# Optimization experiments

Measured on AMD Instinct MI355X. Metric: run time of the kernel, lower is better.

Reference implementation:

```python
import jax, jax.numpy as jnp
import numpy as np

HIDDEN = 1152
HEADS = 16
HEAD_DIM = HIDDEN // HEADS

def setup_inputs() -> dict:
    key = jax.random.key(0)
    ks = jax.random.split(key, 7)
    s = 1.0 / np.sqrt(HIDDEN)
    return {
        "x": jax.random.normal(ks[0], (16, 1024, HIDDEN), dtype=jnp.float32),
        "w_qkv": jax.random.normal(ks[1], (3 * HIDDEN, HIDDEN), dtype=jnp.float32) * s,
        "b_qkv": jax.random.normal(ks[2], (3 * HIDDEN,), dtype=jnp.float32) * 0.01,
        "q_gamma": jnp.ones((HEAD_DIM,), dtype=jnp.float32),
        "k_gamma": jnp.ones((HEAD_DIM,), dtype=jnp.float32),
        "w_proj": jax.random.normal(ks[3], (HIDDEN, HIDDEN), dtype=jnp.float32) * s,
        "b_proj": jax.random.normal(ks[4], (HIDDEN,), dtype=jnp.float32) * 0.01,
    }

def _rmsnorm(t, gamma):
    # normalize over last dim (head_dim); torch RMSNorm default eps = finfo(dtype).eps
    eps = jnp.asarray(jnp.finfo(t.dtype).eps, t.dtype)
    ms = jnp.mean(jnp.square(t), axis=-1, keepdims=True)
    return t * jax.lax.rsqrt(ms + eps) * gamma

def reference(x, w_qkv, b_qkv, q_gamma, k_gamma, w_proj, b_proj):
    B, S, H = x.shape
    qkv = x @ w_qkv.T + b_qkv                       # [B,S,3H]
    qkv = qkv.reshape(B, S, 3, HEADS, HEAD_DIM)
    qkv = jnp.transpose(qkv, (2, 0, 3, 1, 4))       # [3,B,nh,S,hd]
    q, k, v = qkv[0], qkv[1], qkv[2]
    q = _rmsnorm(q, q_gamma)
    k = _rmsnorm(k, k_gamma)
    scale = 1.0 / np.sqrt(HEAD_DIM)
    scores = jnp.einsum('bhqd,bhkd->bhqk', q, k) * scale
    probs = jax.nn.softmax(scores, axis=-1)
    out = jnp.einsum('bhqk,bhkd->bhqd', probs, v)   # [B,nh,S,hd]
    out = jnp.transpose(out, (0, 2, 1, 3)).reshape(B, S, H)
    return out @ w_proj.T + b_proj
```

## Files before the change

kernel.cpp:

```cpp
#include <hip/hip_runtime.h>

typedef _Float16 f16;
typedef _Float16 f16x8 __attribute__((ext_vector_type(8)));
typedef _Float16 f16x4 __attribute__((ext_vector_type(4)));
typedef float f32x4 __attribute__((ext_vector_type(4)));

__device__ __forceinline__ void gld16(const void* g, void* l) {
    __builtin_amdgcn_global_load_lds(
        (const __attribute__((address_space(1))) void*)g,
        (__attribute__((address_space(3))) void*)l,
        16, 0, 0);
}

__global__ __launch_bounds__(256) void f32_to_f16_vec(const float* __restrict__ in,
                                                      f16* __restrict__ out, long n4) {
    long i = (long)blockIdx.x * 256 + threadIdx.x;
    if (i < n4) {
        float4 v = ((const float4*)in)[i];
        f16x4 o = {(f16)v.x, (f16)v.y, (f16)v.z, (f16)v.w};
        ((f16x4*)out)[i] = o;
    }
}

constexpr int GBUF = 24576;

template<int P, int KK, bool STG>
__device__ __forceinline__ void phase_step(f16* sm,
                                           const f16*& gSA, const f16*& gSB,
                                           long sKA, int dA, int dB,
                                           int rA, int rB,
                                           f32x4 (&acc)[4][4]) {
    const f16* ba = sm + P * GBUF + KK * 8192 + rA;
    const f16* bb = sm + P * GBUF + KK * 4096 + rB;
    f16x8 af[4], bf[4];
#pragma unroll
    for (int mt = 0; mt < 4; ++mt) af[mt] = *(const f16x8*)(ba + mt * 512);
#pragma unroll
    for (int nt = 0; nt < 4; ++nt) bf[nt] = *(const f16x8*)(bb + nt * 512);
    if (STG) {
        constexpr int TB = (KK == 0) ? (P ^ 1) : P;
        constexpr int TK = (KK == 0) ? 1 : 0;
        f16* d = sm + TB * GBUF;
        gld16(gSA,       d + TK * 8192 + dA);
        gld16(gSA + sKA, d + TK * 8192 + dA + 512);
        gld16(gSB,       d + 16384 + TK * 4096 + dB);
        gSA += 32; gSB += 32;
    }
    asm volatile("s_waitcnt lgkmcnt(0)" ::: "memory");
    __builtin_amdgcn_sched_barrier(0);
    __builtin_amdgcn_s_setprio(1);
#pragma unroll
    for (int mt = 0; mt < 4; ++mt)
#pragma unroll
        for (int nt = 0; nt < 4; ++nt)
            acc[mt][nt] = __builtin_amdgcn_mfma_f32_16x16x32_f16(
                af[mt], bf[nt], acc[mt][nt], 0, 0, 0);
    __builtin_amdgcn_s_setprio(0);
}

__global__ __launch_bounds__(512, 2) void gemm8(const f16* __restrict__ A,
                                                const f16* __restrict__ B,
                                                const float* __restrict__ bias,
                                                float* __restrict__ Cf,
                                                f16* __restrict__ Ch,
                                                int M, int N, int K) {
    __shared__ f16 sm[2 * GBUF];
    const int tid = threadIdx.x;
    const int w = tid >> 6, lane = tid & 63;
    const int quad = lane >> 4, l16 = lane & 15;
    const int wm = w >> 1, wn = w & 1;

    const int nnb = N >> 7;
    const int mpx = (M >> 8) >> 3;
    const int xcd = blockIdx.x & 7;
    const int s = blockIdx.x >> 3;
    const int mband = s / nnb;
    const int nblk = s - mband * nnb;
    const long m0 = (long)(xcd * mpx + mband) << 8;
    const long n0 = (long)nblk << 7;

    const int r4 = lane >> 2;
    const int scw = ((lane & 3) ^ ((lane >> 3) & 3)) << 3;
    const f16* gSA = A + (m0 + w * 32 + r4) * (long)K + scw;
    const f16* gSB = B + (n0 + w * 16 + r4) * (long)K + scw;
    const long sKA = (long)16 * K;
    const int dA = __builtin_amdgcn_readfirstlane(w * 1024);
    const int dB = __builtin_amdgcn_readfirstlane(w * 512);

    const int swz8 = (quad ^ ((l16 >> 1) & 3)) << 3;
    const int rA = (wm * 64 + l16) * 32 + swz8;
    const int rB = 16384 + (wn * 64 + l16) * 32 + swz8;

    f32x4 acc[4][4] = {};

    gld16(gSA, sm + dA); gld16(gSA + sKA, sm + dA + 512);
    gld16(gSB, sm + 16384 + dB); gSA += 32; gSB += 32;
    gld16(gSA, sm + 8192 + dA); gld16(gSA + sKA, sm + 8192 + dA + 512);
    gld16(gSB, sm + 20480 + dB); gSA += 32; gSB += 32;
    gld16(gSA, sm + GBUF + dA); gld16(gSA + sKA, sm + GBUF + dA + 512);
    gld16(gSB, sm + GBUF + 16384 + dB); gSA += 32; gSB += 32;
    asm volatile("s_waitcnt vmcnt(6)" ::: "memory");
    __builtin_amdgcn_s_barrier();

#define VMB(N) asm volatile("s_waitcnt vmcnt(" #N ")" ::: "memory"); \
               __builtin_amdgcn_s_barrier();

#pragma unroll 1
    for (int it = 0; it < 8; ++it) {
        phase_step<0, 0, true>(sm, gSA, gSB, sKA, dA, dB, rA, rB, acc); VMB(6)
        phase_step<0, 1, true>(sm, gSA, gSB, sKA, dA, dB, rA, rB, acc); VMB(6)
        phase_step<1, 0, true>(sm, gSA, gSB, sKA, dA, dB, rA, rB, acc); VMB(6)
        phase_step<1, 1, true>(sm, gSA, gSB, sKA, dA, dB, rA, rB, acc); VMB(6)
    }
    phase_step<0, 0, true >(sm, gSA, gSB, sKA, dA, dB, rA, rB, acc); VMB(6)
    phase_step<0, 1, false>(sm, gSA, gSB, sKA, dA, dB, rA, rB, acc); VMB(3)
    phase_step<1, 0, false>(sm, gSA, gSB, sKA, dA, dB, rA, rB, acc); VMB(0)
    phase_step<1, 1, false>(sm, gSA, gSB, sKA, dA, dB, rA, rB, acc);
#undef VMB

    float bv[4];
#pragma unroll
    for (int nt = 0; nt < 4; ++nt)
        bv[nt] = bias ? bias[n0 + wn * 64 + nt * 16 + l16] : 0.f;
#pragma unroll
    for (int mt = 0; mt < 4; ++mt) {
#pragma unroll
        for (int r = 0; r < 4; ++r) {
            const long row = m0 + wm * 64 + mt * 16 + quad * 4 + r;
#pragma unroll
            for (int nt = 0; nt < 4; ++nt) {
                const long col = n0 + wn * 64 + nt * 16 + l16;
                const float v = acc[mt][nt][r] + bv[nt];
                if (Ch) Ch[row * (long)N + col] = (f16)v;
                else    Cf[row * (long)N + col] = v;
            }
        }
    }
}

__global__ __launch_bounds__(256) void qk_norm2(f16* __restrict__ qkv,
                                                const float* __restrict__ qg,
                                                const float* __restrict__ kg,
                                                f16* __restrict__ kc) {
    const float QSCALE = 0.117851130198f;
    const int t = blockIdx.x * 256 + threadIdx.x;
    const int h = t & 15;
    const long bs = t >> 4;
    f16* qp = qkv + bs * 3456 + h * 72;
    {
        f16x8 v[9];
        float ss = 0.f;
#pragma unroll
        for (int c = 0; c < 9; ++c) {
            v[c] = *(const f16x8*)(qp + c * 8);
#pragma unroll
            for (int j = 0; j < 8; ++j) { float f = (float)v[c][j]; ss += f * f; }
        }
        const float rs = rsqrtf(ss * (1.f / 72.f) + 1.1920928955078125e-7f) * QSCALE;
#pragma unroll
        for (int c = 0; c < 9; ++c) {
            f16x8 o;
#pragma unroll
            for (int j = 0; j < 8; ++j) o[j] = (f16)((float)v[c][j] * rs * qg[c * 8 + j]);
            *(f16x8*)(qp + c * 8) = o;
        }
    }
    {
        const f16* kp = qp + 1152;
        f16* dst = kc + ((long)((bs >> 10) * 16 + h) * 1024 + (bs & 1023)) * 72;
        f16x8 v[9];
        float ss = 0.f;
#pragma unroll
        for (int c = 0; c < 9; ++c) {
            v[c] = *(const f16x8*)(kp + c * 8);
#pragma unroll
            for (int j = 0; j < 8; ++j) { float f = (float)v[c][j]; ss += f * f; }
        }
        const float rs = rsqrtf(ss * (1.f / 72.f) + 1.1920928955078125e-7f);
#pragma unroll
        for (int c = 0; c < 9; ++c) {
            f16x8 o;
#pragma unroll
            for (int j = 0; j < 8; ++j) o[j] = (f16)((float)v[c][j] * rs * kg[c * 8 + j]);
            *(f16x8*)(dst + c * 8) = o;
        }
    }
}

__global__ __launch_bounds__(256) void vt_kernel(const f16* __restrict__ QKV,
                                                 f16* __restrict__ Vt) {
    __shared__ f16 tile[64][73];
    const int tid = threadIdx.x;
    const int bh = blockIdx.x;
    const int b = bh >> 4, h = bh & 15;
    const int s0 = blockIdx.y * 64;
    for (int idx = tid; idx < 64 * 72; idx += 256) {
        const int r = idx / 72, c = idx % 72;
        tile[r][c] = QKV[((long)(b * 1024 + s0 + r)) * 3456 + 2304 + h * 72 + c];
    }
    __syncthreads();
    for (int idx = tid; idx < 72 * 64; idx += 256) {
        const int d = idx >> 6, s = idx & 63;
        Vt[((long)bh * 72 + d) * 1024 + s0 + s] = tile[s][d];
    }
}

__global__ __launch_bounds__(256) void attn2(const f16* __restrict__ QKV,
                                             const f16* __restrict__ Kc,
                                             const f16* __restrict__ Vt,
                                             f16* __restrict__ O) {
    constexpr int S = 1024;
    __shared__ f16 smem[64 * 72 + 80 * 76];
    f16* Ks = smem;
    f16* Vs = smem + 64 * 72;
    const int tid = threadIdx.x;
    const int w = tid >> 6, lane = tid & 63;
    const int quad = lane >> 4, l16 = lane & 15;

    const int b = blockIdx.x;
    const int xcd = b & 7;
    const int j = b >> 3;
    const int bh = ((j >> 3) << 3) | xcd;
    const int qt = j & 7;
    const int bb = bh >> 4, h = bh & 15;
    const int q0 = qt * 128;

    for (int i = tid; i < 8 * 76; i += 256) {
        const int pr = i / 76, pc = i % 76;
        Vs[(72 + pr) * 76 + pc] = (pr == 0 && pc < 64) ? (f16)1.f : (f16)0.f;
    }

    const f16* qrow0 = QKV + ((long)(bb * 1024 + q0 + w * 32 + l16)) * 3456 + h * 72;
    const f16* qrow1 = qrow0 + (long)16 * 3456;
    f16x8 qz = {};
    f16x8 qf[2][3];
    qf[0][0] = *(const f16x8*)(qrow0 + quad * 8);
    qf[0][1] = *(const f16x8*)(qrow0 + 32 + quad * 8);
    qf[0][2] = (quad == 0) ? *(const f16x8*)(qrow0 + 64) : qz;
    qf[1][0] = *(const f16x8*)(qrow1 + quad * 8);
    qf[1][1] = *(const f16x8*)(qrow1 + 32 + quad * 8);
    qf[1][2] = (quad == 0) ? *(const f16x8*)(qrow1 + 64) : qz;

    f32x4 o[2][5] = {};

    const f16* gK = Kc + (long)bh * S * 72;
    const f16* gV = Vt + (long)bh * 72 * S;

    for (int s0 = 0; s0 < S; s0 += 64) {
        for (int ch = w; ch < 9; ch += 4)
            gld16(gK + (long)s0 * 72 + ch * 512 + lane * 8,
                  &Ks[__builtin_amdgcn_readfirstlane(ch * 512)]);
#pragma unroll
        for (int it = 0; it < 3; ++it) {
            const int idx = it * 256 + tid;
            if (idx < 576) {
                const int d = idx >> 3, s8 = (idx & 7) * 8;
                f16x8 v = *(const f16x8*)(gV + (long)d * 1024 + s0 + s8);
                f16x4 lo = {v[0], v[1], v[2], v[3]};
                f16x4 hi = {v[4], v[5], v[6], v[7]};
                *(f16x4*)&Vs[d * 76 + s8] = lo;
                *(f16x4*)&Vs[d * 76 + s8 + 4] = hi;
            }
        }
        __syncthreads();

        f32x4 sc[4][2] = {};
#pragma unroll
        for (int ss = 0; ss < 4; ++ss) {
            const int base = (ss * 16 + l16) * 72;
            f16x8 k0 = *(const f16x8*)&Ks[base + quad * 8];
            f16x8 k1 = *(const f16x8*)&Ks[base + 32 + quad * 8];
            f16x8 k2 = *(const f16x8*)&Ks[base + 64 + quad * 8];
            sc[ss][0] = __builtin_amdgcn_mfma_f32_16x16x32_f16(k0, qf[0][0], sc[ss][0], 0, 0, 0);
            sc[ss][0] = __builtin_amdgcn_mfma_f32_16x16x32_f16(k1, qf[0][1], sc[ss][0], 0, 0, 0);
            sc[ss][0] = __builtin_amdgcn_mfma_f32_16x16x32_f16(k2, qf[0][2], sc[ss][0], 0, 0, 0);
            sc[ss][1] = __builtin_amdgcn_mfma_f32_16x16x32_f16(k0, qf[1][0], sc[ss][1], 0, 0, 0);
            sc[ss][1] = __builtin_amdgcn_mfma_f32_16x16x32_f16(k1, qf[1][1], sc[ss][1], 0, 0, 0);
            sc[ss][1] = __builtin_amdgcn_mfma_f32_16x16x32_f16(k2, qf[1][2], sc[ss][1], 0, 0, 0);
        }

        f16x4 pf[4][2];
#pragma unroll
        for (int ss = 0; ss < 4; ++ss)
#pragma unroll
            for (int qs = 0; qs < 2; ++qs) {
                f16x4 pk;
#pragma unroll
                for (int r = 0; r < 4; ++r) pk[r] = (f16)__expf(sc[ss][qs][r]);
                pf[ss][qs] = pk;
            }

#pragma unroll
        for (int vt = 0; vt < 5; ++vt) {
#pragma unroll
            for (int ss = 0; ss < 4; ++ss) {
                f16x4 vf = *(const f16x4*)&Vs[(vt * 16 + l16) * 76 + ss * 16 + quad * 4];
                o[0][vt] = __builtin_amdgcn_mfma_f32_16x16x16f16(vf, pf[ss][0], o[0][vt], 0, 0, 0);
                o[1][vt] = __builtin_amdgcn_mfma_f32_16x16x16f16(vf, pf[ss][1], o[1][vt], 0, 0, 0);
            }
        }
        __syncthreads();
    }

    const float l0 = __shfl(o[0][4][0], 32 + l16);
    const float l1 = __shfl(o[1][4][0], 32 + l16);
    const float inv[2] = {1.f / l0, 1.f / l1};

    f16* es = smem + w * 2560;
#pragma unroll
    for (int qs = 0; qs < 2; ++qs) {
        f16* row = es + (qs * 16 + l16) * 80;
#pragma unroll
        for (int vt = 0; vt < 5; ++vt)
#pragma unroll
            for (int r = 0; r < 4; ++r) {
                const int d = vt * 16 + quad * 4 + r;
                if (d < 72) row[d] = (f16)(o[qs][vt][r] * inv[qs]);
            }
    }
    const long rowbase = (long)bb * 1024 + q0 + w * 32;
#pragma unroll
    for (int it = 0; it < 5; ++it) {
        const int idx = it * 64 + lane;
        if (idx < 288) {
            const int q = idx / 9, c = idx - q * 9;
            f16x4 a = *(const f16x4*)&es[q * 80 + c * 8];
            f16x4 b2 = *(const f16x4*)&es[q * 80 + c * 8 + 4];
            f16* dst = O + (rowbase + q) * 1152 + h * 72 + c * 8;
            *(f16x4*)dst = a;
            *(f16x4*)(dst + 4) = b2;
        }
    }
}

extern "C" void kernel_launch(void* const* d_in, const int* in_sizes, int n_in,
                              void* d_out, int out_size, void* d_ws, size_t ws_size,
                              hipStream_t stream) {
    const float* x       = (const float*)d_in[0];
    const float* w_qkv   = (const float*)d_in[1];
    const float* b_qkv   = (const float*)d_in[2];
    const float* q_gamma = (const float*)d_in[3];
    const float* k_gamma = (const float*)d_in[4];
    const float* w_proj  = (const float*)d_in[5];
    const float* b_proj  = (const float*)d_in[6];
    float* out = (float*)d_out;

    char* p = (char*)d_ws;
    f16* x_h = (f16*)p;      p += (size_t)16384 * 1152 * 2;
    f16* wqkv_h = (f16*)p;   p += (size_t)3456 * 1152 * 2;
    f16* wproj_h = (f16*)p;  p += (size_t)1152 * 1152 * 2;
    f16* qkv_h = (f16*)p;    p += (size_t)16384 * 3456 * 2;
    const size_t needed = (size_t)(p - (char*)d_ws);
    if (ws_size < needed) return;

    f16* k_c = (f16*)d_out;
    f16* v_t = (f16*)d_out + (size_t)16384 * 1152;

    f32_to_f16_vec<<<18432, 256, 0, stream>>>(x, x_h, 16384L * 1152 / 4);
    f32_to_f16_vec<<<3888, 256, 0, stream>>>(w_qkv, wqkv_h, 3456L * 1152 / 4);
    f32_to_f16_vec<<<1296, 256, 0, stream>>>(w_proj, wproj_h, 1152L * 1152 / 4);

    gemm8<<<1728, 512, 0, stream>>>(
        x_h, wqkv_h, b_qkv, nullptr, qkv_h, 16384, 3456, 1152);

    qk_norm2<<<1024, 256, 0, stream>>>(qkv_h, q_gamma, k_gamma, k_c);
    vt_kernel<<<dim3(256, 16), 256, 0, stream>>>(qkv_h, v_t);

    attn2<<<2048, 256, 0, stream>>>(qkv_h, k_c, v_t, x_h );

    gemm8<<<576, 512, 0, stream>>>(
        x_h, wproj_h, b_proj, out, nullptr, 16384, 1152, 1152);
}
```

Baseline: 528.0 us.

## Enlarge GEMM tile to 512x128 with triple-buffered LDS pipeline

The GEMM block tile grows from 256x128 to 512x128: each wave now computes 128x64 using 8x4 accumulators, and the grid sizes are halved to match. The two-buffer, two-half-K staging is replaced by a three-buffer ring of 32-wide K slices. Each step splits its MFMA work into two halves separated by barriers so the B fragments can be reused across both A halves. This aims to raise arithmetic intensity and cut global and LDS traffic per FLOP. The costs are fewer blocks (occupancy drops from 2 blocks per CU to 1), higher register pressure, and extra barriers.

```diff
diff --git a/kernel.cpp b/kernel.cpp
--- a/kernel.cpp
+++ b/kernel.cpp
@@ -22,30 +22,26 @@
     }
 }
 
-constexpr int GBUF = 24576;
-
-template<int P, int KK, bool STG>
-__device__ __forceinline__ void phase_step(f16* sm,
-                                           const f16*& gSA, const f16*& gSB,
-                                           long sKA, int dA, int dB,
-                                           int rA, int rB,
-                                           f32x4 (&acc)[4][4]) {
-    const f16* ba = sm + P * GBUF + KK * 8192 + rA;
-    const f16* bb = sm + P * GBUF + KK * 4096 + rB;
-    f16x8 af[4], bf[4];
-#pragma unroll
-    for (int mt = 0; mt < 4; ++mt) af[mt] = *(const f16x8*)(ba + mt * 512);
-#pragma unroll
-    for (int nt = 0; nt < 4; ++nt) bf[nt] = *(const f16x8*)(bb + nt * 512);
+constexpr int BUFE = 20480;
+
+template<int BUF, bool STG>
+__device__ __forceinline__ void kstep(f16* sm,
+                                      const f16*& gA, const f16*& gB, long k16,
+                                      int dA, int dB, int rA, int rB,
+                                      f32x4 (&acc)[8][4]) {
+    const f16* bp = sm + BUF * BUFE;
+    f16* tb = sm + ((BUF + 2) % 3) * BUFE;
+    f16x8 bf[4], af[4];
+#pragma unroll
+    for (int nt = 0; nt < 4; ++nt) bf[nt] = *(const f16x8*)(bp + rB + nt * 512);
+#pragma unroll
+    for (int mt = 0; mt < 4; ++mt) af[mt] = *(const f16x8*)(bp + rA + mt * 512);
     if (STG) {
-        constexpr int TB = (KK == 0) ? (P ^ 1) : P;
-        constexpr int TK = (KK == 0) ? 1 : 0;
-        f16* d = sm + TB * GBUF;
-        gld16(gSA,       d + TK * 8192 + dA);
-        gld16(gSA + sKA, d + TK * 8192 + dA + 512);
-        gld16(gSB,       d + 16384 + TK * 4096 + dB);
-        gSA += 32; gSB += 32;
-    }
+        gld16(gA,       tb + dA);
+        gld16(gA + k16, tb + dA + 512);
+        gld16(gB,       tb + 16384 + dB);
+    }
+    __builtin_amdgcn_s_barrier();
     asm volatile("s_waitcnt lgkmcnt(0)" ::: "memory");
     __builtin_amdgcn_sched_barrier(0);
     __builtin_amdgcn_s_setprio(1);
@@ -56,66 +52,88 @@
             acc[mt][nt] = __builtin_amdgcn_mfma_f32_16x16x32_f16(
                 af[mt], bf[nt], acc[mt][nt], 0, 0, 0);
     __builtin_amdgcn_s_setprio(0);
-}
-
-__global__ __launch_bounds__(512, 2) void gemm8(const f16* __restrict__ A,
-                                                const f16* __restrict__ B,
-                                                const float* __restrict__ bias,
-                                                float* __restrict__ Cf,
-                                                f16* __restrict__ Ch,
-                                                int M, int N, int K) {
-    __shared__ f16 sm[2 * GBUF];
+    __builtin_amdgcn_s_barrier();
+    f16x8 ah[4];
+#pragma unroll
+    for (int mt = 0; mt < 4; ++mt) ah[mt] = *(const f16x8*)(bp + rA + 2048 + mt * 512);
+    if (STG) {
+        gld16(gA + 2 * k16, tb + dA + 1024);
+        gld16(gA + 3 * k16, tb + dA + 1536);
+        gA += 32; gB += 32;
+    }
+    __builtin_amdgcn_s_barrier();
+    asm volatile("s_waitcnt lgkmcnt(0)" ::: "memory");
+    __builtin_amdgcn_sched_barrier(0);
+    __builtin_amdgcn_s_setprio(1);
+#pragma unroll
+    for (int mt = 0; mt < 4; ++mt)
+#pragma unroll
+        for (int nt = 0; nt < 4; ++nt)
+            acc[4 + mt][nt] = __builtin_amdgcn_mfma_f32_16x16x32_f16(
+                ah[mt], bf[nt], acc[4 + mt][nt], 0, 0, 0);
+    __builtin_amdgcn_s_setprio(0);
+}
+
+__global__ __launch_bounds__(512) void gemm8(const f16* __restrict__ A,
+                                             const f16* __restrict__ B,
+                                             const float* __restrict__ bias,
+                                             float* __restrict__ Cf,
+                                             f16* __restrict__ Ch,
+                                             int M, int N, int K) {
+    __shared__ f16 sm[3 * BUFE];
     const int tid = threadIdx.x;
     const int w = tid >> 6, lane = tid & 63;
     const int quad = lane >> 4, l16 = lane & 15;
     const int wm = w >> 1, wn = w & 1;
 
     const int nnb = N >> 7;
-    const int mpx = (M >> 8) >> 3;
+    const int mpx = (M >> 9) >> 3;
     const int xcd = blockIdx.x & 7;
     const int s = blockIdx.x >> 3;
     const int mband = s / nnb;
     const int nblk = s - mband * nnb;
-    const long m0 = (long)(xcd * mpx + mband) << 8;
+    const long m0 = (long)(xcd * mpx + mband) << 9;
     const long n0 = (long)nblk << 7;
 
     const int r4 = lane >> 2;
     const int scw = ((lane & 3) ^ ((lane >> 3) & 3)) << 3;
-    const f16* gSA = A + (m0 + w * 32 + r4) * (long)K + scw;
-    const f16* gSB = B + (n0 + w * 16 + r4) * (long)K + scw;
-    const long sKA = (long)16 * K;
-    const int dA = __builtin_amdgcn_readfirstlane(w * 1024);
+    const f16* gA = A + (m0 + w * 64 + r4) * (long)K + scw;
+    const f16* gB = B + (n0 + w * 16 + r4) * (long)K + scw;
+    const long k16 = (long)16 * K;
+    const int dA = __builtin_amdgcn_readfirstlane(w * 2048);
     const int dB = __builtin_amdgcn_readfirstlane(w * 512);
 
     const int swz8 = (quad ^ ((l16 >> 1) & 3)) << 3;
-    const int rA = (wm * 64 + l16) * 32 + swz8;
+    const int rA = (wm * 128 + l16) * 32 + swz8;
     const int rB = 16384 + (wn * 64 + l16) * 32 + swz8;
 
-    f32x4 acc[4][4] = {};
-
-    gld16(gSA, sm + dA); gld16(gSA + sKA, sm + dA + 512);
-    gld16(gSB, sm + 16384 + dB); gSA += 32; gSB += 32;
-    gld16(gSA, sm + 8192 + dA); gld16(gSA + sKA, sm + 8192 + dA + 512);
-    gld16(gSB, sm + 20480 + dB); gSA += 32; gSB += 32;
-    gld16(gSA, sm + GBUF + dA); gld16(gSA + sKA, sm + GBUF + dA + 512);
-    gld16(gSB, sm + GBUF + 16384 + dB); gSA += 32; gSB += 32;
-    asm volatile("s_waitcnt vmcnt(6)" ::: "memory");
+    f32x4 acc[8][4] = {};
+
+#pragma unroll
+    for (int tt = 0; tt < 2; ++tt) {
+        f16* d = sm + tt * BUFE;
+        gld16(gA,           d + dA);
+        gld16(gA + k16,     d + dA + 512);
+        gld16(gA + 2 * k16, d + dA + 1024);
+        gld16(gA + 3 * k16, d + dA + 1536);
+        gld16(gB,           d + 16384 + dB);
+        gA += 32; gB += 32;
+    }
+    asm volatile("s_waitcnt vmcnt(5)" ::: "memory");
     __builtin_amdgcn_s_barrier();
 
 #define VMB(N) asm volatile("s_waitcnt vmcnt(" #N ")" ::: "memory"); \
                __builtin_amdgcn_s_barrier();
 
 #pragma unroll 1
-    for (int it = 0; it < 8; ++it) {
-        phase_step<0, 0, true>(sm, gSA, gSB, sKA, dA, dB, rA, rB, acc); VMB(6)
-        phase_step<0, 1, true>(sm, gSA, gSB, sKA, dA, dB, rA, rB, acc); VMB(6)
-        phase_step<1, 0, true>(sm, gSA, gSB, sKA, dA, dB, rA, rB, acc); VMB(6)
-        phase_step<1, 1, true>(sm, gSA, gSB, sKA, dA, dB, rA, rB, acc); VMB(6)
-    }
-    phase_step<0, 0, true >(sm, gSA, gSB, sKA, dA, dB, rA, rB, acc); VMB(6)
-    phase_step<0, 1, false>(sm, gSA, gSB, sKA, dA, dB, rA, rB, acc); VMB(3)
-    phase_step<1, 0, false>(sm, gSA, gSB, sKA, dA, dB, rA, rB, acc); VMB(0)
-    phase_step<1, 1, false>(sm, gSA, gSB, sKA, dA, dB, rA, rB, acc);
+    for (int it = 0; it < 11; ++it) {
+        kstep<0, true>(sm, gA, gB, k16, dA, dB, rA, rB, acc); VMB(5)
+        kstep<1, true>(sm, gA, gB, k16, dA, dB, rA, rB, acc); VMB(5)
+        kstep<2, true>(sm, gA, gB, k16, dA, dB, rA, rB, acc); VMB(5)
+    }
+    kstep<0, true >(sm, gA, gB, k16, dA, dB, rA, rB, acc); VMB(5)
+    kstep<1, false>(sm, gA, gB, k16, dA, dB, rA, rB, acc); VMB(0)
+    kstep<2, false>(sm, gA, gB, k16, dA, dB, rA, rB, acc);
 #undef VMB
 
     float bv[4];
@@ -123,10 +141,10 @@
     for (int nt = 0; nt < 4; ++nt)
         bv[nt] = bias ? bias[n0 + wn * 64 + nt * 16 + l16] : 0.f;
 #pragma unroll
-    for (int mt = 0; mt < 4; ++mt) {
+    for (int mt = 0; mt < 8; ++mt) {
 #pragma unroll
         for (int r = 0; r < 4; ++r) {
-            const long row = m0 + wm * 64 + mt * 16 + quad * 4 + r;
+            const long row = m0 + wm * 128 + mt * 16 + quad * 4 + r;
 #pragma unroll
             for (int nt = 0; nt < 4; ++nt) {
                 const long col = n0 + wn * 64 + nt * 16 + l16;
@@ -360,7 +378,7 @@
     f32_to_f16_vec<<<3888, 256, 0, stream>>>(w_qkv, wqkv_h, 3456L * 1152 / 4);
     f32_to_f16_vec<<<1296, 256, 0, stream>>>(w_proj, wproj_h, 1152L * 1152 / 4);
 
-    gemm8<<<1728, 512, 0, stream>>>(
+    gemm8<<<864, 512, 0, stream>>>(
         x_h, wqkv_h, b_qkv, nullptr, qkv_h, 16384, 3456, 1152);
 
     qk_norm2<<<1024, 256, 0, stream>>>(qkv_h, q_gamma, k_gamma, k_c);
@@ -368,6 +386,6 @@
 
     attn2<<<2048, 256, 0, stream>>>(qkv_h, k_c, v_t, x_h );
 
-    gemm8<<<576, 512, 0, stream>>>(
+    gemm8<<<288, 512, 0, stream>>>(
         x_h, wproj_h, b_proj, out, nullptr, 16384, 1152, 1152);
 }
```

Measured after the change: 574.4 us. +8.8%, slower.
